# Performance work log

Hardware: AMD Instinct MI355X
Metric: run time of the kernel (lower is better)

The kernel has to match this reference:

```python
import jax, jax.numpy as jnp
import numpy as np


def lsigf_db(h, S, x, b):
    """Time-varying delayed graph filter (LSIGF_DB).
    h: (F, E, K, G) filter taps; S: (B, T, E, N, N) batch time-varying GSO;
    x: (B, T, G, N) node signals; b: (F, 1) bias or None.
    Diffusion recursion: x_k(t) = x_{k-1}(t-1) @ S(t)  (zero signal before t=0).
    """
    K = h.shape[2]
    B, T, E, N, _ = S.shape
    G = x.shape[2]
    xk = jnp.broadcast_to(x[:, :, None], (B, T, E, G, N))  # k = 0 tap
    zs = [xk]
    for _ in range(1, K):
        # delay one time step: x(t-1), zero-padded at t=0
        xk = jnp.concatenate([jnp.zeros_like(xk[:, :1]), xk[:, :-1]], axis=1)
        # shift by current GSO: matmul(x, S) as in the torch implementation
        xk = jnp.einsum('btegm,btemn->btegn', xk, S)
        zs.append(xk)
    z = jnp.stack(zs, axis=2)  # (B, T, K, E, G, N)
    y = jnp.einsum('fekg,btkegn->btfn', h, z)  # (B, T, F, N)
    if b is not None:
        y = y + b[None, None]  # (F,1) broadcasts over nodes
    return y


def setup_inputs() -> dict:
    key = jax.random.key(0)
    ks = jax.random.split(key, 12)
    B, T, E, N = 8, 64, 1, 256
    F0, F1, F2 = 12, 64, 32
    K1, K2 = 3, 3
    R1, R2 = 32, 2

    def u(k, shape, fan):
        s = 1.0 / np.sqrt(fan)
        return jax.random.uniform(k, shape, jnp.float32, -s, s)

    return {
        'x': jax.random.normal(ks[0], (B, T, F0, N), jnp.float32),
        'S': jax.random.normal(ks[1], (B, T, E, N, N), jnp.float32),
        'W1': u(ks[2], (F1, E, K1, F0), F0 * K1),
        'b1': u(ks[3], (F1, 1), F0 * K1),
        'W2': u(ks[4], (F2, E, K2, F1), F1 * K2),
        'b2': u(ks[5], (F2, 1), F1 * K2),
        'A1': u(ks[6], (R1, F2), F2),
        'c1': u(ks[7], (R1,), F2),
        'A2': u(ks[8], (R2, R1), R1),
        'c2': u(ks[9], (R2,), R1),
    }


def reference(x, S, W1, b1, W2, b2, A1, c1, A2, c2):
    # Graph filtering layers (GraphFilter_DB + Tanh)
    y = jnp.tanh(lsigf_db(W1, S, x, b1))
    y = jnp.tanh(lsigf_db(W2, S, y, b2))
    # Local readout: per-node MLP Linear -> Tanh -> Linear
    y = jnp.swapaxes(y, 2, 3)  # (B, T, N, F2)
    y = jnp.tanh(y @ A1.T + c1)
    y = y @ A2.T + c2
    return jnp.swapaxes(y, 2, 3)  # (B, T, dimReadout[-1], N)
```

## Files before the change

### kernel.cpp

```cpp
#include <hip/hip_runtime.h>
#include <hip/hip_fp16.h>

typedef _Float16 half8 __attribute__((ext_vector_type(8)));
typedef _Float16 half4v __attribute__((ext_vector_type(4)));
typedef float f32x4 __attribute__((ext_vector_type(4)));

static constexpr int B_ = 8, T_ = 64, N_ = 256;
static constexpr int F0 = 12, F1 = 64, F2 = 32;
static constexpr int BT_ = B_ * T_;
static constexpr size_t STPK_BT = (size_t)N_ * 32 * 16;

__device__ inline float tanh_fast(float x) {
    x = fminf(20.f, fmaxf(-20.f, x));
    float e = __expf(2.f * x);
    return (e - 1.f) / (e + 1.f);
}

__global__ __launch_bounds__(256) void k_transpose_u1(
    const float* __restrict__ S, const float* __restrict__ x,
    _Float16* __restrict__ STpk,
    _Float16* __restrict__ U1h, _Float16* __restrict__ U1l,
    _Float16* __restrict__ U1Th, _Float16* __restrict__ U1Tl) {
    __shared__ float tile[64][129];
    int bt = blockIdx.x;
    int t  = bt & (T_ - 1);
    int n0 = blockIdx.y * 64;
    const float* s = S + (size_t)bt * N_ * N_;
    _Float16* stpk = STpk + (size_t)bt * STPK_BT;
    int tid = threadIdx.x;
    int q  = tid & 15, r0  = tid >> 4;
    int q2 = tid & 7,  nr0 = tid >> 3;
    int lane = tid & 63, wv = tid >> 6;
    int l15 = lane & 15, lk = lane >> 4;
    const float* A = x + (size_t)(bt - 1) * F0 * N_;
    f32x4 acc = (f32x4){0.f, 0.f, 0.f, 0.f};

    for (int m0 = 0; m0 < N_; m0 += 128) {
        f32x4 vbuf[8];
        #pragma unroll
        for (int ii = 0; ii < 8; ++ii) {
            int rr = r0 + ii * 16;
            vbuf[ii] = __builtin_nontemporal_load(
                (const f32x4*)(s + (size_t)(m0 + rr) * N_ + n0 + q * 4));
        }
        #pragma unroll
        for (int ii = 0; ii < 8; ++ii) {
            int rr = r0 + ii * 16;
            tile[q * 4 + 0][rr] = vbuf[ii][0];
            tile[q * 4 + 1][rr] = vbuf[ii][1];
            tile[q * 4 + 2][rr] = vbuf[ii][2];
            tile[q * 4 + 3][rr] = vbuf[ii][3];
        }
        __syncthreads();
        #pragma unroll
        for (int nn = nr0; nn < 64; nn += 32) {
            #pragma unroll
            for (int ci = 0; ci < 2; ++ci) {
                int mc = ci * 8 + q2;
                half8 h, l;
                #pragma unroll
                for (int e = 0; e < 8; ++e) {
                    float v = tile[nn][mc * 8 + e];
                    _Float16 hh = (_Float16)v;
                    h[e] = hh;
                    l[e] = (_Float16)(v - (float)hh);
                }
                size_t o = ((size_t)(n0 + nn) * 32 + (m0 >> 3) + mc) * 16;
                *(half8*)(stpk + o) = h;
                *(half8*)(stpk + o + 8) = l;
            }
        }
        if (t > 0) {
            #pragma unroll
            for (int kkl = 0; kkl < 4; ++kkl) {
                int ml = kkl * 32 + lk * 8;
                half8 ah = {}, al = {};
                if (l15 < F0) {
                    const float* ar = A + (size_t)l15 * N_ + m0 + ml;
                    float4 v0 = *(const float4*)(ar);
                    float4 v1 = *(const float4*)(ar + 4);
                    float vv[8] = {v0.x, v0.y, v0.z, v0.w, v1.x, v1.y, v1.z, v1.w};
                    #pragma unroll
                    for (int c = 0; c < 8; ++c) {
                        _Float16 hh = (_Float16)vv[c];
                        ah[c] = hh;
                        al[c] = (_Float16)(vv[c] - (float)hh);
                    }
                }
                half8 bh, bl;
                const float* tr = &tile[wv * 16 + l15][ml];
                #pragma unroll
                for (int e = 0; e < 8; ++e) {
                    float v = tr[e];
                    _Float16 hh = (_Float16)v;
                    bh[e] = hh;
                    bl[e] = (_Float16)(v - (float)hh);
                }
                acc = __builtin_amdgcn_mfma_f32_16x16x32_f16(ah, bh, acc, 0, 0, 0);
                acc = __builtin_amdgcn_mfma_f32_16x16x32_f16(al, bh, acc, 0, 0, 0);
                acc = __builtin_amdgcn_mfma_f32_16x16x32_f16(ah, bl, acc, 0, 0, 0);
            }
        }
        __syncthreads();
    }
    {
        int n = n0 + wv * 16 + l15;
        _Float16* O_h = U1h + (size_t)bt * 16 * N_;
        _Float16* O_l = U1l + (size_t)bt * 16 * N_;
        half4v th, tl;
        #pragma unroll
        for (int r = 0; r < 4; ++r) {
            float v = acc[r];
            _Float16 h = (_Float16)v;
            _Float16 lo = (_Float16)(v - (float)h);
            O_h[(size_t)(lk * 4 + r) * N_ + n] = h;
            O_l[(size_t)(lk * 4 + r) * N_ + n] = lo;
            th[r] = h;
            tl[r] = lo;
        }
        size_t to = ((size_t)bt * N_ + n) * 16 + lk * 4;
        *(half4v*)(U1Th + to) = th;
        *(half4v*)(U1Tl + to) = tl;
    }
}

__global__ void k_transpose_x(const float* __restrict__ x,
                              _Float16* __restrict__ XTh, _Float16* __restrict__ XTl) {
    int bt = blockIdx.x;
    int n = threadIdx.x;
    const float* xc = x + (size_t)bt * F0 * N_;
    half8 hb[2] = {}, lb[2] = {};
    #pragma unroll
    for (int g = 0; g < F0; ++g) {
        float v = xc[(size_t)g * N_ + n];
        _Float16 hh = (_Float16)v;
        hb[g >> 3][g & 7] = hh;
        lb[g >> 3][g & 7] = (_Float16)(v - (float)hh);
    }
    size_t o = ((size_t)bt * N_ + n) * 16;
    *(half8*)(XTh + o) = hb[0];
    *(half8*)(XTh + o + 8) = hb[1];
    *(half8*)(XTl + o) = lb[0];
    *(half8*)(XTl + o + 8) = lb[1];
}

__global__ void k_chainV1(const _Float16* __restrict__ Ah, const _Float16* __restrict__ Al,
                          const _Float16* __restrict__ STpk,
                          _Float16* __restrict__ OTh, _Float16* __restrict__ OTl) {
    int bt = blockIdx.x;
    int t = bt & (T_ - 1);
    int wave = threadIdx.x >> 6;
    int lane = threadIdx.x & 63;
    int l15 = lane & 15;
    int lk = lane >> 4;
    int n0 = blockIdx.y * 128 + wave * 32;

    f32x4 acc[2];
    #pragma unroll
    for (int j = 0; j < 2; ++j) acc[j] = (f32x4){0.f, 0.f, 0.f, 0.f};

    if (t > 0) {
        const _Float16* A_h = Ah + (size_t)(bt - 1) * 16 * N_;
        const _Float16* A_l = Al + (size_t)(bt - 1) * 16 * N_;
        const _Float16* Bp = STpk + (size_t)bt * STPK_BT;
        #pragma unroll
        for (int kk = 0; kk < 8; ++kk) {
            int kof = kk * 32 + lk * 8;
            half8 ah = *(const half8*)(A_h + (size_t)l15 * N_ + kof);
            half8 al = *(const half8*)(A_l + (size_t)l15 * N_ + kof);
            #pragma unroll
            for (int j = 0; j < 2; ++j) {
                size_t bb = ((size_t)(n0 + j * 16 + l15) * 32 + kk * 4 + lk) * 16;
                half8 bh = *(const half8*)(Bp + bb);
                half8 bl = *(const half8*)(Bp + bb + 8);
                acc[j] = __builtin_amdgcn_mfma_f32_16x16x32_f16(ah, bh, acc[j], 0, 0, 0);
                acc[j] = __builtin_amdgcn_mfma_f32_16x16x32_f16(al, bh, acc[j], 0, 0, 0);
                acc[j] = __builtin_amdgcn_mfma_f32_16x16x32_f16(ah, bl, acc[j], 0, 0, 0);
            }
        }
    }
    #pragma unroll
    for (int j = 0; j < 2; ++j) {
        half4v th, tl;
        #pragma unroll
        for (int r = 0; r < 4; ++r) {
            float v = acc[j][r];
            _Float16 h = (_Float16)v;
            th[r] = h;
            tl[r] = (_Float16)(v - (float)h);
        }
        size_t to = ((size_t)bt * N_ + n0 + j * 16 + l15) * 16 + lk * 4;
        *(half4v*)(OTh + to) = th;
        *(half4v*)(OTl + to) = tl;
    }
}

__global__ void k_combine1(const _Float16* __restrict__ XTh, const _Float16* __restrict__ XTl,
                           const _Float16* __restrict__ U1Th, const _Float16* __restrict__ U1Tl,
                           const _Float16* __restrict__ V1Th, const _Float16* __restrict__ V1Tl,
                           const float* __restrict__ W1, const float* __restrict__ b1,
                           _Float16* __restrict__ Y1Th, _Float16* __restrict__ Y1Tl) {
    __shared__ _Float16 wh[64 * 72], wl[64 * 72];
    int bt = blockIdx.x;
    int tid = threadIdx.x;
    for (int i = tid; i < 64 * 72; i += 256) {
        int f = i / 72, k = i % 72;
        float v = 0.f;
        if (k < 12) v = W1[f * 36 + k];
        else if (k >= 16 && k < 28) v = W1[f * 36 + 12 + (k - 16)];
        else if (k >= 32 && k < 44) v = W1[f * 36 + 24 + (k - 32)];
        _Float16 hh = (_Float16)v;
        wh[i] = hh;
        wl[i] = (_Float16)(v - (float)hh);
    }
    __syncthreads();

    int wv = tid >> 6, lane = tid & 63, l15 = lane & 15, lk = lane >> 4;
    int n0 = wv * 64;
    f32x4 acc[4][4];
    #pragma unroll
    for (int i = 0; i < 4; ++i)
        #pragma unroll
        for (int j = 0; j < 4; ++j) acc[i][j] = (f32x4){0.f, 0.f, 0.f, 0.f};

    #pragma unroll
    for (int kk = 0; kk < 2; ++kk) {
        half8 bh[4], bl[4];
        #pragma unroll
        for (int j = 0; j < 4; ++j) {
            size_t base16 = ((size_t)bt * N_ + n0 + j * 16 + l15) * 16;
            if (kk == 0) {
                if (lk < 2) {
                    bh[j] = *(const half8*)(XTh + base16 + lk * 8);
                    bl[j] = *(const half8*)(XTl + base16 + lk * 8);
                } else {
                    bh[j] = *(const half8*)(U1Th + base16 + (lk - 2) * 8);
                    bl[j] = *(const half8*)(U1Tl + base16 + (lk - 2) * 8);
                }
            } else {
                if (lk < 2) {
                    bh[j] = *(const half8*)(V1Th + base16 + lk * 8);
                    bl[j] = *(const half8*)(V1Tl + base16 + lk * 8);
                } else {
                    bh[j] = half8{};
                    bl[j] = half8{};
                }
            }
        }
        #pragma unroll
        for (int i = 0; i < 4; ++i) {
            half8 ah = *(const half8*)(wh + (i * 16 + l15) * 72 + kk * 32 + lk * 8);
            half8 al = *(const half8*)(wl + (i * 16 + l15) * 72 + kk * 32 + lk * 8);
            #pragma unroll
            for (int j = 0; j < 4; ++j) {
                acc[i][j] = __builtin_amdgcn_mfma_f32_16x16x32_f16(ah, bh[j], acc[i][j], 0, 0, 0);
                acc[i][j] = __builtin_amdgcn_mfma_f32_16x16x32_f16(al, bh[j], acc[i][j], 0, 0, 0);
                acc[i][j] = __builtin_amdgcn_mfma_f32_16x16x32_f16(ah, bl[j], acc[i][j], 0, 0, 0);
            }
        }
    }
    #pragma unroll
    for (int i = 0; i < 4; ++i) {
        float bb[4];
        #pragma unroll
        for (int r = 0; r < 4; ++r) bb[r] = b1[i * 16 + lk * 4 + r];
        #pragma unroll
        for (int j = 0; j < 4; ++j) {
            half4v th, tl;
            #pragma unroll
            for (int r = 0; r < 4; ++r) {
                float yv = tanh_fast(acc[i][j][r] + bb[r]);
                _Float16 h = (_Float16)yv;
                th[r] = h;
                tl[r] = (_Float16)(yv - (float)h);
            }
            size_t to = ((size_t)bt * N_ + n0 + j * 16 + l15) * 64 + i * 16 + lk * 4;
            *(half4v*)(Y1Th + to) = th;
            *(half4v*)(Y1Tl + to) = tl;
        }
    }
}

__global__ void k_proj(const _Float16* __restrict__ Y1Th, const _Float16* __restrict__ Y1Tl,
                       const float* __restrict__ W2,
                       _Float16* __restrict__ Gh, _Float16* __restrict__ Gl,
                       float* __restrict__ Hf, float* __restrict__ Y2a) {
    __shared__ _Float16 wh[96 * 72], wl[96 * 72];
    int bt = blockIdx.x;
    int tid = threadIdx.x;
    for (int i = tid; i < 96 * 64; i += 256) {
        int r = i >> 6, g = i & 63;
        int f, off;
        if (r < 32)      { f = r;      off = 128; }
        else if (r < 64) { f = r - 32; off = 64;  }
        else             { f = r - 64; off = 0;   }
        float v = W2[f * 192 + off + g];
        _Float16 hh = (_Float16)v;
        wh[r * 72 + g] = hh;
        wl[r * 72 + g] = (_Float16)(v - (float)hh);
    }
    __syncthreads();

    int wv = tid >> 6, lane = tid & 63, l15 = lane & 15, lk = lane >> 4;
    int n0 = wv * 64;
    f32x4 acc[6][4];
    #pragma unroll
    for (int i = 0; i < 6; ++i)
        #pragma unroll
        for (int j = 0; j < 4; ++j) acc[i][j] = (f32x4){0.f, 0.f, 0.f, 0.f};

    const _Float16* Bh = Y1Th + (size_t)bt * N_ * 64;
    const _Float16* Bl = Y1Tl + (size_t)bt * N_ * 64;
    #pragma unroll
    for (int kk = 0; kk < 2; ++kk) {
        int kof = kk * 32 + lk * 8;
        half8 bh[4], bl[4];
        #pragma unroll
        for (int j = 0; j < 4; ++j) {
            bh[j] = *(const half8*)(Bh + (size_t)(n0 + j * 16 + l15) * 64 + kof);
            bl[j] = *(const half8*)(Bl + (size_t)(n0 + j * 16 + l15) * 64 + kof);
        }
        #pragma unroll
        for (int i = 0; i < 6; ++i) {
            half8 ah = *(const half8*)(wh + (i * 16 + l15) * 72 + kof);
            half8 al = *(const half8*)(wl + (i * 16 + l15) * 72 + kof);
            #pragma unroll
            for (int j = 0; j < 4; ++j) {
                acc[i][j] = __builtin_amdgcn_mfma_f32_16x16x32_f16(ah, bh[j], acc[i][j], 0, 0, 0);
                acc[i][j] = __builtin_amdgcn_mfma_f32_16x16x32_f16(al, bh[j], acc[i][j], 0, 0, 0);
                acc[i][j] = __builtin_amdgcn_mfma_f32_16x16x32_f16(ah, bl[j], acc[i][j], 0, 0, 0);
            }
        }
    }
    #pragma unroll
    for (int i = 0; i < 6; ++i)
        #pragma unroll
        for (int j = 0; j < 4; ++j)
            #pragma unroll
            for (int r = 0; r < 4; ++r) {
                int row = i * 16 + lk * 4 + r;
                int col = n0 + j * 16 + l15;
                float v = acc[i][j][r];
                if (row < 32) {
                    _Float16 hh = (_Float16)v;
                    size_t o = ((size_t)bt * 32 + row) * N_ + col;
                    Gh[o] = hh;
                    Gl[o] = (_Float16)(v - (float)hh);
                } else if (row < 64) {
                    Hf[((size_t)bt * 32 + row - 32) * N_ + col] = v;
                } else {
                    Y2a[((size_t)bt * 32 + row - 64) * N_ + col] = v;
                }
            }
}

__global__ void k_chainR(const _Float16* __restrict__ Gh, const _Float16* __restrict__ Gl,
                         const _Float16* __restrict__ STpk,
                         const float* __restrict__ Hf,
                         _Float16* __restrict__ Rh, _Float16* __restrict__ Rl) {
    int bt = blockIdx.x;
    int t = bt & (T_ - 1);
    int wave = threadIdx.x >> 6;
    int lane = threadIdx.x & 63;
    int l15 = lane & 15;
    int lk = lane >> 4;
    int n0 = blockIdx.y * 128 + wave * 32;

    f32x4 acc[2][2];
    #pragma unroll
    for (int i = 0; i < 2; ++i)
        #pragma unroll
        for (int j = 0; j < 2; ++j) acc[i][j] = (f32x4){0.f, 0.f, 0.f, 0.f};

    if (t > 0) {
        const _Float16* A_h = Gh + (size_t)(bt - 1) * 32 * N_;
        const _Float16* A_l = Gl + (size_t)(bt - 1) * 32 * N_;
        const _Float16* Bp = STpk + (size_t)bt * STPK_BT;
        #pragma unroll
        for (int kk = 0; kk < 8; ++kk) {
            int kof = kk * 32 + lk * 8;
            half8 ah[2], al[2];
            #pragma unroll
            for (int i = 0; i < 2; ++i) {
                ah[i] = *(const half8*)(A_h + (size_t)(i * 16 + l15) * N_ + kof);
                al[i] = *(const half8*)(A_l + (size_t)(i * 16 + l15) * N_ + kof);
            }
            #pragma unroll
            for (int j = 0; j < 2; ++j) {
                size_t bb = ((size_t)(n0 + j * 16 + l15) * 32 + kk * 4 + lk) * 16;
                half8 bh = *(const half8*)(Bp + bb);
                half8 bl = *(const half8*)(Bp + bb + 8);
                #pragma unroll
                for (int i = 0; i < 2; ++i) {
                    acc[i][j] = __builtin_amdgcn_mfma_f32_16x16x32_f16(ah[i], bh, acc[i][j], 0, 0, 0);
                    acc[i][j] = __builtin_amdgcn_mfma_f32_16x16x32_f16(al[i], bh, acc[i][j], 0, 0, 0);
                    acc[i][j] = __builtin_amdgcn_mfma_f32_16x16x32_f16(ah[i], bl, acc[i][j], 0, 0, 0);
                }
            }
        }
    }
    const float* Hb = Hf + (size_t)bt * 32 * N_;
    _Float16* R_h = Rh + (size_t)bt * 32 * N_;
    _Float16* R_l = Rl + (size_t)bt * 32 * N_;
    #pragma unroll
    for (int i = 0; i < 2; ++i)
        #pragma unroll
        for (int j = 0; j < 2; ++j)
            #pragma unroll
            for (int r = 0; r < 4; ++r) {
                size_t idx = (size_t)(i * 16 + lk * 4 + r) * N_ + n0 + j * 16 + l15;
                float v = acc[i][j][r] + Hb[idx];
                _Float16 h = (_Float16)v;
                R_h[idx] = h;
                R_l[idx] = (_Float16)(v - (float)h);
            }
}

__global__ void k_chainY2(const _Float16* __restrict__ Rh, const _Float16* __restrict__ Rl,
                          const _Float16* __restrict__ STpk,
                          const float* __restrict__ Y2a, const float* __restrict__ b2,
                          const float* __restrict__ A1, const float* __restrict__ c1,
                          const float* __restrict__ A2, const float* __restrict__ c2,
                          float* __restrict__ out) {
    __shared__ float y2s[32 * 133];
    __shared__ float la1[32 * 33];
    int bt = blockIdx.x;
    int t = bt & (T_ - 1);
    int tid = threadIdx.x;
    for (int i = tid; i < 32 * 32; i += 256) la1[(i >> 5) * 33 + (i & 31)] = A1[i];

    int wave = tid >> 6;
    int lane = tid & 63;
    int l15 = lane & 15;
    int lk = lane >> 4;
    int n0 = blockIdx.y * 128 + wave * 32;

    f32x4 acc[2][2];
    #pragma unroll
    for (int i = 0; i < 2; ++i)
        #pragma unroll
        for (int j = 0; j < 2; ++j) acc[i][j] = (f32x4){0.f, 0.f, 0.f, 0.f};

    if (t > 0) {
        const _Float16* A_h = Rh + (size_t)(bt - 1) * 32 * N_;
        const _Float16* A_l = Rl + (size_t)(bt - 1) * 32 * N_;
        const _Float16* Bp = STpk + (size_t)bt * STPK_BT;
        #pragma unroll
        for (int kk = 0; kk < 8; ++kk) {
            int kof = kk * 32 + lk * 8;
            half8 ah[2], al[2];
            #pragma unroll
            for (int i = 0; i < 2; ++i) {
                ah[i] = *(const half8*)(A_h + (size_t)(i * 16 + l15) * N_ + kof);
                al[i] = *(const half8*)(A_l + (size_t)(i * 16 + l15) * N_ + kof);
            }
            #pragma unroll
            for (int j = 0; j < 2; ++j) {
                size_t bb = ((size_t)(n0 + j * 16 + l15) * 32 + kk * 4 + lk) * 16;
                half8 bh = *(const half8*)(Bp + bb);
                half8 bl = *(const half8*)(Bp + bb + 8);
                #pragma unroll
                for (int i = 0; i < 2; ++i) {
                    acc[i][j] = __builtin_amdgcn_mfma_f32_16x16x32_f16(ah[i], bh, acc[i][j], 0, 0, 0);
                    acc[i][j] = __builtin_amdgcn_mfma_f32_16x16x32_f16(al[i], bh, acc[i][j], 0, 0, 0);
                    acc[i][j] = __builtin_amdgcn_mfma_f32_16x16x32_f16(ah[i], bl, acc[i][j], 0, 0, 0);
                }
            }
        }
    }
    const float* Ya = Y2a + (size_t)bt * 32 * N_;
    int colb0 = wave * 32;
    #pragma unroll
    for (int i = 0; i < 2; ++i)
        #pragma unroll
        for (int j = 0; j < 2; ++j)
            #pragma unroll
            for (int r = 0; r < 4; ++r) {
                int row = i * 16 + lk * 4 + r;
                int colb = colb0 + j * 16 + l15;
                int n = blockIdx.y * 128 + colb;
                y2s[row * 133 + colb] = acc[i][j][r] + Ya[(size_t)row * N_ + n] + b2[row];
            }
    __syncthreads();

    if (tid < 128) {
        int colb = tid;
        int n = blockIdx.y * 128 + colb;
        float y2v[32];
        #pragma unroll
        for (int f = 0; f < 32; ++f) y2v[f] = tanh_fast(y2s[f * 133 + colb]);
        float o0 = 0.f, o1 = 0.f;
        #pragma unroll
        for (int j = 0; j < 32; ++j) {
            const float* a1r = la1 + j * 33;
            float s = c1[j];
            #pragma unroll
            for (int f = 0; f < 32; ++f) s += a1r[f] * y2v[f];
            float hj = tanh_fast(s);
            o0 += A2[j] * hj;
            o1 += A2[32 + j] * hj;
        }
        out[((size_t)bt * 2 + 0) * N_ + n] = o0 + c2[0];
        out[((size_t)bt * 2 + 1) * N_ + n] = o1 + c2[1];
    }
}

extern "C" void kernel_launch(void* const* d_in, const int* in_sizes, int n_in,
                              void* d_out, int out_size, void* d_ws, size_t ws_size,
                              hipStream_t stream) {
    const float* x  = (const float*)d_in[0];
    const float* S  = (const float*)d_in[1];
    const float* W1 = (const float*)d_in[2];
    const float* b1 = (const float*)d_in[3];
    const float* W2 = (const float*)d_in[4];
    const float* b2 = (const float*)d_in[5];
    const float* A1 = (const float*)d_in[6];
    const float* c1 = (const float*)d_in[7];
    const float* A2 = (const float*)d_in[8];
    const float* c2 = (const float*)d_in[9];
    float* out = (float*)d_out;

    char* ws = (char*)d_ws;
    const size_t SZ_STPK = (size_t)BT_ * STPK_BT * 2;
    const size_t SZ_Y1T = (size_t)BT_ * N_ * 64 * 2;
    const size_t SZ_G   = (size_t)BT_ * 32 * N_ * 2;
    const size_t SZ_H   = (size_t)BT_ * 32 * N_ * 4;
    const size_t SZ_T16 = (size_t)BT_ * N_ * 16 * 2;
    size_t off = 0;
    _Float16* STpk = (_Float16*)(ws + off); off += SZ_STPK;
    _Float16* Y1Th = (_Float16*)(ws + off); off += SZ_Y1T;
    _Float16* Y1Tl = (_Float16*)(ws + off); off += SZ_Y1T;
    _Float16* Gh   = (_Float16*)(ws + off); off += SZ_G;
    _Float16* Gl   = (_Float16*)(ws + off); off += SZ_G;
    float*    Hf   = (float*)(ws + off); off += SZ_H;
    float*    Y2a  = (float*)(ws + off); off += SZ_H;
    _Float16* Rh   = (_Float16*)(ws + off); off += SZ_G;
    _Float16* Rl   = (_Float16*)(ws + off); off += SZ_G;
    if (ws_size < off) return;

    _Float16* XTh  = (_Float16*)Hf;
    _Float16* XTl  = XTh + SZ_T16 / 2;
    _Float16* U1Th = (_Float16*)Y2a;
    _Float16* U1Tl = U1Th + SZ_T16 / 2;
    _Float16* V1Th = U1Tl + SZ_T16 / 2;
    _Float16* V1Tl = V1Th + SZ_T16 / 2;
    _Float16* U1h  = Rh;
    _Float16* U1l  = Rl;

    k_transpose_u1<<<dim3(BT_, 4), 256, 0, stream>>>(S, x, STpk,
                                                     U1h, U1l, U1Th, U1Tl);
    k_transpose_x<<<BT_, 256, 0, stream>>>(x, XTh, XTl);
    k_chainV1<<<dim3(BT_, 2), 256, 0, stream>>>(U1h, U1l, STpk, V1Th, V1Tl);
    k_combine1<<<BT_, 256, 0, stream>>>(XTh, XTl, U1Th, U1Tl, V1Th, V1Tl, W1, b1, Y1Th, Y1Tl);
    k_proj<<<BT_, 256, 0, stream>>>(Y1Th, Y1Tl, W2, Gh, Gl, Hf, Y2a);
    k_chainR<<<dim3(BT_, 2), 256, 0, stream>>>(Gh, Gl, STpk, Hf, Rh, Rl);
    k_chainY2<<<dim3(BT_, 2), 256, 0, stream>>>(Rh, Rl, STpk, Y2a, b2,
                                                A1, c1, A2, c2, out);
}
```

Baseline: 228.4 us.

## Drop pre-packed fp16 S buffer; transpose and split S on the fly per chain kernel

Removes the precomputed transposed hi/lo fp16 copy of S that the first kernel wrote and the three chain kernels read. Each chain kernel now loads fp32 S tiles directly, transposes them through shared memory, and splits them into hi/lo halves in registers before the MFMAs. This cuts the large packed-S write and keeps one pass over S per chain kernel instead of reading a packed copy. The cost is repeated fp32 S reads in three kernels, extra conversion ALU work, and block-wide syncs in the inner loop. Aliased workspace buffers are also given their own space.

```diff
diff --git a/kernel.cpp b/kernel.cpp
--- a/kernel.cpp
+++ b/kernel.cpp
@@ -8,7 +8,6 @@
 static constexpr int B_ = 8, T_ = 64, N_ = 256;
 static constexpr int F0 = 12, F1 = 64, F2 = 32;
 static constexpr int BT_ = B_ * T_;
-static constexpr size_t STPK_BT = (size_t)N_ * 32 * 16;
 
 __device__ inline float tanh_fast(float x) {
     x = fminf(20.f, fmaxf(-20.f, x));
@@ -16,9 +15,8 @@
     return (e - 1.f) / (e + 1.f);
 }
 
-__global__ __launch_bounds__(256) void k_transpose_u1(
+__global__ __launch_bounds__(256) void k_u1(
     const float* __restrict__ S, const float* __restrict__ x,
-    _Float16* __restrict__ STpk,
     _Float16* __restrict__ U1h, _Float16* __restrict__ U1l,
     _Float16* __restrict__ U1Th, _Float16* __restrict__ U1Tl) {
     __shared__ float tile[64][129];
@@ -26,10 +24,8 @@
     int t  = bt & (T_ - 1);
     int n0 = blockIdx.y * 64;
     const float* s = S + (size_t)bt * N_ * N_;
-    _Float16* stpk = STpk + (size_t)bt * STPK_BT;
     int tid = threadIdx.x;
     int q  = tid & 15, r0  = tid >> 4;
-    int q2 = tid & 7,  nr0 = tid >> 3;
     int lane = tid & 63, wv = tid >> 6;
     int l15 = lane & 15, lk = lane >> 4;
     const float* A = x + (size_t)(bt - 1) * F0 * N_;
@@ -40,8 +36,7 @@
         #pragma unroll
         for (int ii = 0; ii < 8; ++ii) {
             int rr = r0 + ii * 16;
-            vbuf[ii] = __builtin_nontemporal_load(
-                (const f32x4*)(s + (size_t)(m0 + rr) * N_ + n0 + q * 4));
+            vbuf[ii] = *(const f32x4*)(s + (size_t)(m0 + rr) * N_ + n0 + q * 4);
         }
         #pragma unroll
         for (int ii = 0; ii < 8; ++ii) {
@@ -52,24 +47,6 @@
             tile[q * 4 + 3][rr] = vbuf[ii][3];
         }
         __syncthreads();
-        #pragma unroll
-        for (int nn = nr0; nn < 64; nn += 32) {
-            #pragma unroll
-            for (int ci = 0; ci < 2; ++ci) {
-                int mc = ci * 8 + q2;
-                half8 h, l;
-                #pragma unroll
-                for (int e = 0; e < 8; ++e) {
-                    float v = tile[nn][mc * 8 + e];
-                    _Float16 hh = (_Float16)v;
-                    h[e] = hh;
-                    l[e] = (_Float16)(v - (float)hh);
-                }
-                size_t o = ((size_t)(n0 + nn) * 32 + (m0 >> 3) + mc) * 16;
-                *(half8*)(stpk + o) = h;
-                *(half8*)(stpk + o + 8) = l;
-            }
-        }
         if (t > 0) {
             #pragma unroll
             for (int kkl = 0; kkl < 4; ++kkl) {
@@ -145,15 +122,17 @@
 }
 
 __global__ void k_chainV1(const _Float16* __restrict__ Ah, const _Float16* __restrict__ Al,
-                          const _Float16* __restrict__ STpk,
+                          const float* __restrict__ S,
                           _Float16* __restrict__ OTh, _Float16* __restrict__ OTl) {
+    __shared__ float tile[128][65];
     int bt = blockIdx.x;
     int t = bt & (T_ - 1);
-    int wave = threadIdx.x >> 6;
-    int lane = threadIdx.x & 63;
-    int l15 = lane & 15;
-    int lk = lane >> 4;
-    int n0 = blockIdx.y * 128 + wave * 32;
+    int tid = threadIdx.x;
+    int nq = tid & 31, mr = tid >> 5;
+    int wave = tid >> 6, lane = tid & 63;
+    int l15 = lane & 15, lk = lane >> 4;
+    int nb0 = blockIdx.y * 128;
+    int n0 = nb0 + wave * 32;
 
     f32x4 acc[2];
     #pragma unroll
@@ -162,21 +141,41 @@
     if (t > 0) {
         const _Float16* A_h = Ah + (size_t)(bt - 1) * 16 * N_;
         const _Float16* A_l = Al + (size_t)(bt - 1) * 16 * N_;
-        const _Float16* Bp = STpk + (size_t)bt * STPK_BT;
-        #pragma unroll
-        for (int kk = 0; kk < 8; ++kk) {
-            int kof = kk * 32 + lk * 8;
-            half8 ah = *(const half8*)(A_h + (size_t)l15 * N_ + kof);
-            half8 al = *(const half8*)(A_l + (size_t)l15 * N_ + kof);
-            #pragma unroll
-            for (int j = 0; j < 2; ++j) {
-                size_t bb = ((size_t)(n0 + j * 16 + l15) * 32 + kk * 4 + lk) * 16;
-                half8 bh = *(const half8*)(Bp + bb);
-                half8 bl = *(const half8*)(Bp + bb + 8);
-                acc[j] = __builtin_amdgcn_mfma_f32_16x16x32_f16(ah, bh, acc[j], 0, 0, 0);
-                acc[j] = __builtin_amdgcn_mfma_f32_16x16x32_f16(al, bh, acc[j], 0, 0, 0);
-                acc[j] = __builtin_amdgcn_mfma_f32_16x16x32_f16(ah, bl, acc[j], 0, 0, 0);
-            }
+        const float* Sb = S + (size_t)bt * N_ * N_;
+        for (int mc = 0; mc < 4; ++mc) {
+            int m0 = mc * 64;
+            #pragma unroll
+            for (int ii = 0; ii < 8; ++ii) {
+                int rr = mr + ii * 8;
+                f32x4 v = *(const f32x4*)(Sb + (size_t)(m0 + rr) * N_ + nb0 + nq * 4);
+                tile[nq * 4 + 0][rr] = v[0];
+                tile[nq * 4 + 1][rr] = v[1];
+                tile[nq * 4 + 2][rr] = v[2];
+                tile[nq * 4 + 3][rr] = v[3];
+            }
+            __syncthreads();
+            #pragma unroll
+            for (int kk = 0; kk < 2; ++kk) {
+                int kof = m0 + kk * 32 + lk * 8;
+                half8 ah = *(const half8*)(A_h + (size_t)l15 * N_ + kof);
+                half8 al = *(const half8*)(A_l + (size_t)l15 * N_ + kof);
+                #pragma unroll
+                for (int j = 0; j < 2; ++j) {
+                    const float* tr = &tile[wave * 32 + j * 16 + l15][kk * 32 + lk * 8];
+                    half8 bh, bl;
+                    #pragma unroll
+                    for (int e = 0; e < 8; ++e) {
+                        float v = tr[e];
+                        _Float16 hh = (_Float16)v;
+                        bh[e] = hh;
+                        bl[e] = (_Float16)(v - (float)hh);
+                    }
+                    acc[j] = __builtin_amdgcn_mfma_f32_16x16x32_f16(ah, bh, acc[j], 0, 0, 0);
+                    acc[j] = __builtin_amdgcn_mfma_f32_16x16x32_f16(al, bh, acc[j], 0, 0, 0);
+                    acc[j] = __builtin_amdgcn_mfma_f32_16x16x32_f16(ah, bl, acc[j], 0, 0, 0);
+                }
+            }
+            __syncthreads();
         }
     }
     #pragma unroll
@@ -355,16 +354,18 @@
 }
 
 __global__ void k_chainR(const _Float16* __restrict__ Gh, const _Float16* __restrict__ Gl,
-                         const _Float16* __restrict__ STpk,
+                         const float* __restrict__ S,
                          const float* __restrict__ Hf,
                          _Float16* __restrict__ Rh, _Float16* __restrict__ Rl) {
+    __shared__ float tile[128][65];
     int bt = blockIdx.x;
     int t = bt & (T_ - 1);
-    int wave = threadIdx.x >> 6;
-    int lane = threadIdx.x & 63;
-    int l15 = lane & 15;
-    int lk = lane >> 4;
-    int n0 = blockIdx.y * 128 + wave * 32;
+    int tid = threadIdx.x;
+    int nq = tid & 31, mr = tid >> 5;
+    int wave = tid >> 6, lane = tid & 63;
+    int l15 = lane & 15, lk = lane >> 4;
+    int nb0 = blockIdx.y * 128;
+    int n0 = nb0 + wave * 32;
 
     f32x4 acc[2][2];
     #pragma unroll
@@ -375,28 +376,48 @@
     if (t > 0) {
         const _Float16* A_h = Gh + (size_t)(bt - 1) * 32 * N_;
         const _Float16* A_l = Gl + (size_t)(bt - 1) * 32 * N_;
-        const _Float16* Bp = STpk + (size_t)bt * STPK_BT;
-        #pragma unroll
-        for (int kk = 0; kk < 8; ++kk) {
-            int kof = kk * 32 + lk * 8;
-            half8 ah[2], al[2];
-            #pragma unroll
-            for (int i = 0; i < 2; ++i) {
-                ah[i] = *(const half8*)(A_h + (size_t)(i * 16 + l15) * N_ + kof);
-                al[i] = *(const half8*)(A_l + (size_t)(i * 16 + l15) * N_ + kof);
-            }
-            #pragma unroll
-            for (int j = 0; j < 2; ++j) {
-                size_t bb = ((size_t)(n0 + j * 16 + l15) * 32 + kk * 4 + lk) * 16;
-                half8 bh = *(const half8*)(Bp + bb);
-                half8 bl = *(const half8*)(Bp + bb + 8);
+        const float* Sb = S + (size_t)bt * N_ * N_;
+        for (int mc = 0; mc < 4; ++mc) {
+            int m0 = mc * 64;
+            #pragma unroll
+            for (int ii = 0; ii < 8; ++ii) {
+                int rr = mr + ii * 8;
+                f32x4 v = *(const f32x4*)(Sb + (size_t)(m0 + rr) * N_ + nb0 + nq * 4);
+                tile[nq * 4 + 0][rr] = v[0];
+                tile[nq * 4 + 1][rr] = v[1];
+                tile[nq * 4 + 2][rr] = v[2];
+                tile[nq * 4 + 3][rr] = v[3];
+            }
+            __syncthreads();
+            #pragma unroll
+            for (int kk = 0; kk < 2; ++kk) {
+                int kof = m0 + kk * 32 + lk * 8;
+                half8 ah[2], al[2];
                 #pragma unroll
                 for (int i = 0; i < 2; ++i) {
-                    acc[i][j] = __builtin_amdgcn_mfma_f32_16x16x32_f16(ah[i], bh, acc[i][j], 0, 0, 0);
-                    acc[i][j] = __builtin_amdgcn_mfma_f32_16x16x32_f16(al[i], bh, acc[i][j], 0, 0, 0);
-                    acc[i][j] = __builtin_amdgcn_mfma_f32_16x16x32_f16(ah[i], bl, acc[i][j], 0, 0, 0);
-                }
-            }
+                    ah[i] = *(const half8*)(A_h + (size_t)(i * 16 + l15) * N_ + kof);
+                    al[i] = *(const half8*)(A_l + (size_t)(i * 16 + l15) * N_ + kof);
+                }
+                #pragma unroll
+                for (int j = 0; j < 2; ++j) {
+                    const float* tr = &tile[wave * 32 + j * 16 + l15][kk * 32 + lk * 8];
+                    half8 bh, bl;
+                    #pragma unroll
+                    for (int e = 0; e < 8; ++e) {
+                        float v = tr[e];
+                        _Float16 hh = (_Float16)v;
+                        bh[e] = hh;
+                        bl[e] = (_Float16)(v - (float)hh);
+                    }
+                    #pragma unroll
+                    for (int i = 0; i < 2; ++i) {
+                        acc[i][j] = __builtin_amdgcn_mfma_f32_16x16x32_f16(ah[i], bh, acc[i][j], 0, 0, 0);
+                        acc[i][j] = __builtin_amdgcn_mfma_f32_16x16x32_f16(al[i], bh, acc[i][j], 0, 0, 0);
+                        acc[i][j] = __builtin_amdgcn_mfma_f32_16x16x32_f16(ah[i], bl, acc[i][j], 0, 0, 0);
+                    }
+                }
+            }
+            __syncthreads();
         }
     }
     const float* Hb = Hf + (size_t)bt * 32 * N_;
@@ -417,23 +438,23 @@
 }
 
 __global__ void k_chainY2(const _Float16* __restrict__ Rh, const _Float16* __restrict__ Rl,
-                          const _Float16* __restrict__ STpk,
+                          const float* __restrict__ S,
                           const float* __restrict__ Y2a, const float* __restrict__ b2,
                           const float* __restrict__ A1, const float* __restrict__ c1,
                           const float* __restrict__ A2, const float* __restrict__ c2,
                           float* __restrict__ out) {
-    __shared__ float y2s[32 * 133];
+    __shared__ float tile[128][65];
     __shared__ float la1[32 * 33];
     int bt = blockIdx.x;
     int t = bt & (T_ - 1);
     int tid = threadIdx.x;
     for (int i = tid; i < 32 * 32; i += 256) la1[(i >> 5) * 33 + (i & 31)] = A1[i];
 
-    int wave = tid >> 6;
-    int lane = tid & 63;
-    int l15 = lane & 15;
-    int lk = lane >> 4;
-    int n0 = blockIdx.y * 128 + wave * 32;
+    int nq = tid & 31, mr = tid >> 5;
+    int wave = tid >> 6, lane = tid & 63;
+    int l15 = lane & 15, lk = lane >> 4;
+    int nb0 = blockIdx.y * 128;
+    int n0 = nb0 + wave * 32;
 
     f32x4 acc[2][2];
     #pragma unroll
@@ -444,32 +465,54 @@
     if (t > 0) {
         const _Float16* A_h = Rh + (size_t)(bt - 1) * 32 * N_;
         const _Float16* A_l = Rl + (size_t)(bt - 1) * 32 * N_;
-        const _Float16* Bp = STpk + (size_t)bt * STPK_BT;
-        #pragma unroll
-        for (int kk = 0; kk < 8; ++kk) {
-            int kof = kk * 32 + lk * 8;
-            half8 ah[2], al[2];
-            #pragma unroll
-            for (int i = 0; i < 2; ++i) {
-                ah[i] = *(const half8*)(A_h + (size_t)(i * 16 + l15) * N_ + kof);
-                al[i] = *(const half8*)(A_l + (size_t)(i * 16 + l15) * N_ + kof);
-            }
-            #pragma unroll
-            for (int j = 0; j < 2; ++j) {
-                size_t bb = ((size_t)(n0 + j * 16 + l15) * 32 + kk * 4 + lk) * 16;
-                half8 bh = *(const half8*)(Bp + bb);
-                half8 bl = *(const half8*)(Bp + bb + 8);
+        const float* Sb = S + (size_t)bt * N_ * N_;
+        for (int mc = 0; mc < 4; ++mc) {
+            int m0 = mc * 64;
+            #pragma unroll
+            for (int ii = 0; ii < 8; ++ii) {
+                int rr = mr + ii * 8;
+                f32x4 v = *(const f32x4*)(Sb + (size_t)(m0 + rr) * N_ + nb0 + nq * 4);
+                tile[nq * 4 + 0][rr] = v[0];
+                tile[nq * 4 + 1][rr] = v[1];
+                tile[nq * 4 + 2][rr] = v[2];
+                tile[nq * 4 + 3][rr] = v[3];
+            }
+            __syncthreads();
+            #pragma unroll
+            for (int kk = 0; kk < 2; ++kk) {
+                int kof = m0 + kk * 32 + lk * 8;
+                half8 ah[2], al[2];
                 #pragma unroll
                 for (int i = 0; i < 2; ++i) {
-                    acc[i][j] = __builtin_amdgcn_mfma_f32_16x16x32_f16(ah[i], bh, acc[i][j], 0, 0, 0);
-                    acc[i][j] = __builtin_amdgcn_mfma_f32_16x16x32_f16(al[i], bh, acc[i][j], 0, 0, 0);
-                    acc[i][j] = __builtin_amdgcn_mfma_f32_16x16x32_f16(ah[i], bl, acc[i][j], 0, 0, 0);
-                }
-            }
-        }
-    }
+                    ah[i] = *(const half8*)(A_h + (size_t)(i * 16 + l15) * N_ + kof);
+                    al[i] = *(const half8*)(A_l + (size_t)(i * 16 + l15) * N_ + kof);
+                }
+                #pragma unroll
+                for (int j = 0; j < 2; ++j) {
+                    const float* tr = &tile[wave * 32 + j * 16 + l15][kk * 32 + lk * 8];
+                    half8 bh, bl;
+                    #pragma unroll
+                    for (int e = 0; e < 8; ++e) {
+                        float v = tr[e];
+                        _Float16 hh = (_Float16)v;
+                        bh[e] = hh;
+                        bl[e] = (_Float16)(v - (float)hh);
+                    }
+                    #pragma unroll
+                    for (int i = 0; i < 2; ++i) {
+                        acc[i][j] = __builtin_amdgcn_mfma_f32_16x16x32_f16(ah[i], bh, acc[i][j], 0, 0, 0);
+                        acc[i][j] = __builtin_amdgcn_mfma_f32_16x16x32_f16(al[i], bh, acc[i][j], 0, 0, 0);
+                        acc[i][j] = __builtin_amdgcn_mfma_f32_16x16x32_f16(ah[i], bl, acc[i][j], 0, 0, 0);
+                    }
+                }
+            }
+            __syncthreads();
+        }
+    }
+    float* y2s = &tile[0][0];
     const float* Ya = Y2a + (size_t)bt * 32 * N_;
     int colb0 = wave * 32;
+    __syncthreads();
     #pragma unroll
     for (int i = 0; i < 2; ++i)
         #pragma unroll
@@ -478,14 +521,14 @@
             for (int r = 0; r < 4; ++r) {
                 int row = i * 16 + lk * 4 + r;
                 int colb = colb0 + j * 16 + l15;
-                int n = blockIdx.y * 128 + colb;
+                int n = nb0 + colb;
                 y2s[row * 133 + colb] = acc[i][j][r] + Ya[(size_t)row * N_ + n] + b2[row];
             }
     __syncthreads();
 
     if (tid < 128) {
         int colb = tid;
-        int n = blockIdx.y * 128 + colb;
+        int n = nb0 + colb;
         float y2v[32];
         #pragma unroll
         for (int f = 0; f < 32; ++f) y2v[f] = tanh_fast(y2s[f * 133 + colb]);
@@ -521,13 +564,11 @@
     float* out = (float*)d_out;
 
     char* ws = (char*)d_ws;
-    const size_t SZ_STPK = (size_t)BT_ * STPK_BT * 2;
     const size_t SZ_Y1T = (size_t)BT_ * N_ * 64 * 2;
     const size_t SZ_G   = (size_t)BT_ * 32 * N_ * 2;
     const size_t SZ_H   = (size_t)BT_ * 32 * N_ * 4;
     const size_t SZ_T16 = (size_t)BT_ * N_ * 16 * 2;
     size_t off = 0;
-    _Float16* STpk = (_Float16*)(ws + off); off += SZ_STPK;
     _Float16* Y1Th = (_Float16*)(ws + off); off += SZ_Y1T;
     _Float16* Y1Tl = (_Float16*)(ws + off); off += SZ_Y1T;
     _Float16* Gh   = (_Float16*)(ws + off); off += SZ_G;
@@ -536,24 +577,22 @@
     float*    Y2a  = (float*)(ws + off); off += SZ_H;
     _Float16* Rh   = (_Float16*)(ws + off); off += SZ_G;
     _Float16* Rl   = (_Float16*)(ws + off); off += SZ_G;
+    _Float16* XTh  = (_Float16*)(ws + off); off += SZ_T16;
+    _Float16* XTl  = (_Float16*)(ws + off); off += SZ_T16;
+    _Float16* U1Th = (_Float16*)(ws + off); off += SZ_T16;
+    _Float16* U1Tl = (_Float16*)(ws + off); off += SZ_T16;
+    _Float16* V1Th = (_Float16*)(ws + off); off += SZ_T16;
+    _Float16* V1Tl = (_Float16*)(ws + off); off += SZ_T16;
+    _Float16* U1h  = (_Float16*)(ws + off); off += SZ_T16;
+    _Float16* U1l  = (_Float16*)(ws + off); off += SZ_T16;
     if (ws_size < off) return;
 
-    _Float16* XTh  = (_Float16*)Hf;
-    _Float16* XTl  = XTh + SZ_T16 / 2;
-    _Float16* U1Th = (_Float16*)Y2a;
-    _Float16* U1Tl = U1Th + SZ_T16 / 2;
-    _Float16* V1Th = U1Tl + SZ_T16 / 2;
-    _Float16* V1Tl = V1Th + SZ_T16 / 2;
-    _Float16* U1h  = Rh;
-    _Float16* U1l  = Rl;
-
-    k_transpose_u1<<<dim3(BT_, 4), 256, 0, stream>>>(S, x, STpk,
-                                                     U1h, U1l, U1Th, U1Tl);
+    k_u1<<<dim3(BT_, 4), 256, 0, stream>>>(S, x, U1h, U1l, U1Th, U1Tl);
     k_transpose_x<<<BT_, 256, 0, stream>>>(x, XTh, XTl);
-    k_chainV1<<<dim3(BT_, 2), 256, 0, stream>>>(U1h, U1l, STpk, V1Th, V1Tl);
+    k_chainV1<<<dim3(BT_, 2), 256, 0, stream>>>(U1h, U1l, S, V1Th, V1Tl);
     k_combine1<<<BT_, 256, 0, stream>>>(XTh, XTl, U1Th, U1Tl, V1Th, V1Tl, W1, b1, Y1Th, Y1Tl);
     k_proj<<<BT_, 256, 0, stream>>>(Y1Th, Y1Tl, W2, Gh, Gl, Hf, Y2a);
-    k_chainR<<<dim3(BT_, 2), 256, 0, stream>>>(Gh, Gl, STpk, Hf, Rh, Rl);
-    k_chainY2<<<dim3(BT_, 2), 256, 0, stream>>>(Rh, Rl, STpk, Y2a, b2,
+    k_chainR<<<dim3(BT_, 2), 256, 0, stream>>>(Gh, Gl, S, Hf, Rh, Rl);
+    k_chainY2<<<dim3(BT_, 2), 256, 0, stream>>>(Rh, Rl, S, Y2a, b2,
                                                 A1, c1, A2, c2, out);
 }
```

Measured after the change: 198.4 us. 1.15x faster.
